# Kernel optimization log

Hardware: AMD Instinct MI355X
Metric: run time of the kernel (lower is better)

Reference implementation:

```python
import jax, jax.numpy as jnp
import numpy as np

N, R, T = 40000, 2000, 500000   # node_size, rel_size, triple_size
D, DEPTH, PROXY_N = 128, 2, 64  # node_F, depth, proxy rows
DC = D * (DEPTH + 1)            # 384


def _unique_edges(rng, n_rows, n_cols, n_edges):
    # sorted, duplicate-free edge list -> matches torch.sparse coalesce() ordering
    keys = np.unique(rng.integers(0, n_rows * n_cols, size=int(n_edges * 1.05), dtype=np.int64))[:n_edges]
    assert keys.shape[0] == n_edges
    return np.stack([keys // n_cols, keys % n_cols], axis=1)


def _init_emb(key, r, c):
    w = jax.random.normal(key, (r, c), dtype=jnp.float32)
    return w / jnp.maximum(jnp.linalg.norm(w, axis=1, keepdims=True), 1e-12)


def setup_inputs() -> dict:
    rng = np.random.default_rng(0)
    adj = jnp.asarray(_unique_edges(rng, N, N, T))                    # [T,2] (src, dst)
    idx = jnp.stack([jnp.arange(T), jnp.asarray(rng.integers(0, R, T, dtype=np.int64))], axis=1)  # [T,2]
    val = jnp.ones((T,), jnp.float32)
    ent_m = jnp.asarray(_unique_edges(rng, N, N, T))
    rel_m = jnp.asarray(_unique_edges(rng, N, R, T))
    ks = jax.random.split(jax.random.key(0), 12)
    return {
        "ent_emb": _init_emb(ks[0], N, D),
        "rel_emb": _init_emb(ks[1], R, D),
        "e_gate": _init_emb(ks[2], DC, DC),
        "e_proxy": _init_emb(ks[3], PROXY_N, DC),
        "e_bias": _init_emb(ks[4], 1, DC),
        "e_attn": jnp.stack([_init_emb(ks[5], D, 1), _init_emb(ks[6], D, 1)]),
        "r_gate": _init_emb(ks[7], DC, DC),
        "r_proxy": _init_emb(ks[8], PROXY_N, DC),
        "r_bias": _init_emb(ks[9], 1, DC),
        "r_attn": jnp.stack([_init_emb(ks[10], D, 1), _init_emb(ks[11], D, 1)]),
        "val_input": val,
        "adj_input": adj,
        "index_input": idx,
        "ent_matrix": ent_m,
        "rel_matrix": rel_m,
    }


def _l2(x):
    return x / jnp.maximum(jnp.linalg.norm(x, axis=-1, keepdims=True), 1e-12)


def _seg_softmax(v, seg, n):
    m = jax.ops.segment_max(v, seg, num_segments=n)
    e = jnp.exp(v - m[seg])
    s = jax.ops.segment_sum(e, seg, num_segments=n)
    return e / s[seg]


def _adj_agg(edges, emb, n_rows):
    # torch.sparse.softmax over rows of an all-ones adjacency, then sparse @ emb
    rows, cols = edges[:, 0], edges[:, 1]
    w = _seg_softmax(jnp.zeros(edges.shape[0], emb.dtype), rows, n_rows)
    return jax.ops.segment_sum(w[:, None] * emb[cols], rows, num_segments=n_rows)


def _graph_attention(features, rel_emb, edges, sp_idx, sp_val, attn, gate_k, proxy, bias):
    n = features.shape[0]
    t = sp_val.shape[0]
    feats = jnp.tanh(features)
    outs = [feats]
    for l in range(DEPTH):
        # sparse (T,R) @ rel_emb -> per-edge relation embedding, then L2 normalize
        rels_sum = _l2(jax.ops.segment_sum(sp_val[:, None] * rel_emb[sp_idx[:, 1]], sp_idx[:, 0], num_segments=t))
        neighs = feats[edges[:, 1]]                                   # [T,D]
        neighs = neighs - 2.0 * jnp.sum(neighs * rels_sum, axis=1, keepdims=True) * rels_sum  # Householder reflection
        att = _seg_softmax((rels_sum @ attn[l])[:, 0], edges[:, 0], n)  # sparse row softmax
        feats = jnp.tanh(jax.ops.segment_sum(neighs * att[:, None], edges[:, 0], num_segments=n))
        outs.append(feats)
    outputs = jnp.concatenate(outs, axis=1)                           # [N, DC]
    pa = jax.nn.softmax(_l2(outputs) @ _l2(proxy).T, axis=-1)         # [N, 64]
    pf = outputs - pa @ proxy
    gate = jax.nn.sigmoid(pf @ gate_k + bias)
    return gate * outputs + (1.0 - gate) * pf


def reference(ent_emb, rel_emb, e_gate, e_proxy, e_bias, e_attn, r_gate, r_proxy, r_bias, r_attn, val_input, adj_input, index_input, ent_matrix, rel_matrix):
    ent_feature = _adj_agg(ent_matrix, ent_emb, N)                    # [N,D]
    rel_feature = _adj_agg(rel_matrix, rel_emb, N)                    # [N,D]
    out_e = _graph_attention(ent_feature, rel_emb, adj_input, index_input, val_input, e_attn, e_gate, e_proxy, e_bias)
    out_r = _graph_attention(rel_feature, rel_emb, adj_input, index_input, val_input, r_attn, r_gate, r_proxy, r_bias)
    # dropout_rate = 0.0 -> identity
    return jnp.concatenate([out_e, out_r], axis=-1)                   # [N, 2*DC]
```

## Files before the change

kernel.cpp:

```cpp
#include <hip/hip_runtime.h>
#include <hip/hip_fp16.h>


typedef __attribute__((ext_vector_type(4))) float f32x4;
typedef _Float16 h16x2 __attribute__((ext_vector_type(2)));
typedef _Float16 f16x8 __attribute__((ext_vector_type(8)));
typedef float f32x16 __attribute__((ext_vector_type(16)));

__device__ __forceinline__ float wave_sum(float v) {
#pragma unroll
  for (int o = 32; o > 0; o >>= 1) v += __shfl_xor(v, o, 64);
  return v;
}
__device__ __forceinline__ float wave_max(float v) {
#pragma unroll
  for (int o = 32; o > 0; o >>= 1) v = fmaxf(v, __shfl_xor(v, o, 64));
  return v;
}
__device__ __forceinline__ unsigned pkhalf2(float a, float b) {
  __half2 h = __floats2half2_rn(a, b);
  return __builtin_bit_cast(unsigned, h);
}
__device__ __forceinline__ float bcf(unsigned u) {
  return __builtin_bit_cast(float, u);
}
__device__ __forceinline__ unsigned short f2h(float x) {
  return __builtin_bit_cast(unsigned short, (_Float16)x);
}
__device__ __forceinline__ float h2f(unsigned short h) {
  return (float)__builtin_bit_cast(_Float16, h);
}
__device__ __forceinline__ float tanh_fast(float x) {
  float t = __expf(-2.f * fabsf(x));
  float y = (1.f - t) / (1.f + t);
  return copysignf(y, x);
}
__device__ __forceinline__ float fdot2u(unsigned a, unsigned b, float c) {
#if __has_builtin(__builtin_amdgcn_fdot2)
  return __builtin_amdgcn_fdot2(__builtin_bit_cast(h16x2, a),
                                __builtin_bit_cast(h16x2, b), c, false);
#else
  h16x2 x = __builtin_bit_cast(h16x2, a), y = __builtin_bit_cast(h16x2, b);
  return fmaf((float)x.x, (float)y.x, fmaf((float)x.y, (float)y.y, c));
#endif
}

__global__ void rowptr3_kernel(const int* __restrict__ e0,
                               const int* __restrict__ e1,
                               const int* __restrict__ e2, int T, int N,
                               int* __restrict__ p0, int* __restrict__ p1,
                               int* __restrict__ p2) {
  int tid = blockIdx.x * blockDim.x + threadIdx.x;
  int which = tid / (N + 1);
  int r = tid - which * (N + 1);
  if (which >= 3) return;
  const int* E = which == 0 ? e0 : (which == 1 ? e1 : e2);
  int* P = which == 0 ? p0 : (which == 1 ? p1 : p2);
  int lo = 0, hi = T;
  while (lo < hi) {
    int mid = (lo + hi) >> 1;
    if (E[2 * mid] < r) lo = mid + 1; else hi = mid;
  }
  P[r] = lo;
}

__global__ void relprep_kernel(const float* __restrict__ rel_emb,
                               const float* __restrict__ e_attn,
                               const float* __restrict__ r_attn, int R,
                               float* __restrict__ srel,
                               unsigned* __restrict__ rnorm,
                               unsigned* __restrict__ rel16) {
  int r = blockIdx.x * 4 + (threadIdx.x >> 6);
  int lane = threadIdx.x & 63;
  if (r >= R) return;
  float2 v  = *(const float2*)(rel_emb + (size_t)r * 128 + 2 * lane);
  float2 a0 = *(const float2*)(e_attn + 2 * lane);
  float2 a1 = *(const float2*)(e_attn + 128 + 2 * lane);
  float2 b0 = *(const float2*)(r_attn + 2 * lane);
  float2 b1 = *(const float2*)(r_attn + 128 + 2 * lane);
  float n  = wave_sum(v.x * v.x + v.y * v.y);
  float d0 = wave_sum(v.x * a0.x + v.y * a0.y);
  float d1 = wave_sum(v.x * a1.x + v.y * a1.y);
  float d2 = wave_sum(v.x * b0.x + v.y * b0.y);
  float d3 = wave_sum(v.x * b1.x + v.y * b1.y);
  float inv = 1.f / fmaxf(sqrtf(n), 1e-12f);
  rnorm[(size_t)r * 64 + lane] = pkhalf2(v.x * inv, v.y * inv);
  rel16[(size_t)r * 64 + lane] = pkhalf2(v.x, v.y);
  if (lane == 0) {
    srel[r]          = d0 * inv;
    srel[R + r]      = d1 * inv;
    srel[2 * R + r]  = d2 * inv;
    srel[3 * R + r]  = d3 * inv;
  }
}

__global__ void pack_f16_kernel(const float* __restrict__ src,
                                unsigned* __restrict__ dst, int n2) {
  int i = blockIdx.x * blockDim.x + threadIdx.x;
  if (i >= n2) return;
  float2 v = *(const float2*)(src + 2 * (size_t)i);
  dst[i] = pkhalf2(v.x, v.y);
}

__global__ __launch_bounds__(256) void stats_kernel(
    const int* __restrict__ ptr, const int* __restrict__ idx,
    const float* __restrict__ srel, int R, float* __restrict__ stats, int N) {
  int r = blockIdx.x * 4 + (threadIdx.x >> 6);
  if (r >= N) return;
  int lane = threadIdx.x & 63;
  int beg = ptr[r], end = ptr[r + 1];
  const float* s0 = srel;
  const float* s1 = srel + R;
  const float* s2 = srel + 2 * R;
  const float* s3 = srel + 3 * R;
  float m0 = -INFINITY, m1 = -INFINITY, m2 = -INFINITY, m3 = -INFINITY;
  for (int e = beg + lane; e < end; e += 64) {
    int rel = idx[2 * e + 1];
    m0 = fmaxf(m0, s0[rel]); m1 = fmaxf(m1, s1[rel]);
    m2 = fmaxf(m2, s2[rel]); m3 = fmaxf(m3, s3[rel]);
  }
#pragma unroll
  for (int o = 32; o > 0; o >>= 1) {
    m0 = fmaxf(m0, __shfl_xor(m0, o, 64));
    m1 = fmaxf(m1, __shfl_xor(m1, o, 64));
    m2 = fmaxf(m2, __shfl_xor(m2, o, 64));
    m3 = fmaxf(m3, __shfl_xor(m3, o, 64));
  }
  float d0 = 0.f, d1 = 0.f, d2 = 0.f, d3 = 0.f;
  for (int e = beg + lane; e < end; e += 64) {
    int rel = idx[2 * e + 1];
    d0 += __expf(s0[rel] - m0); d1 += __expf(s1[rel] - m1);
    d2 += __expf(s2[rel] - m2); d3 += __expf(s3[rel] - m3);
  }
#pragma unroll
  for (int o = 32; o > 0; o >>= 1) {
    d0 += __shfl_xor(d0, o, 64); d1 += __shfl_xor(d1, o, 64);
    d2 += __shfl_xor(d2, o, 64); d3 += __shfl_xor(d3, o, 64);
  }
  if (lane == 0) {
    float4 a, b;
    a.x = m0; a.y = (d0 > 0.f) ? 1.f / d0 : 0.f;
    a.z = m1; a.w = (d1 > 0.f) ? 1.f / d1 : 0.f;
    b.x = m2; b.y = (d2 > 0.f) ? 1.f / d2 : 0.f;
    b.z = m3; b.w = (d3 > 0.f) ? 1.f / d3 : 0.f;
    *(float4*)(stats + (size_t)r * 8) = a;
    *(float4*)(stats + (size_t)r * 8 + 4) = b;
  }
}

__global__ void weight_kernel(const int* __restrict__ adj,
                              const int* __restrict__ idx,
                              const float* __restrict__ srel, int R,
                              const float* __restrict__ stats,
                              unsigned* __restrict__ pk,
                              uint2* __restrict__ wt0,
                              uint2* __restrict__ wt1, int T) {
  int e = blockIdx.x * blockDim.x + threadIdx.x;
  if (e >= T) return;
  int row = adj[2 * e];
  int col = adj[2 * e + 1];
  int rel = idx[2 * e + 1];
  float4 a = *(const float4*)(stats + (size_t)row * 8);
  float4 b = *(const float4*)(stats + (size_t)row * 8 + 4);
  float w0 = __expf(srel[rel] - a.x) * a.y;
  float w1 = __expf(srel[R + rel] - a.z) * a.w;
  float w2 = __expf(srel[2 * R + rel] - b.x) * b.y;
  float w3 = __expf(srel[3 * R + rel] - b.z) * b.w;
  pk[e] = (unsigned)col | ((unsigned)rel << 16);
  wt0[e] = make_uint2(__builtin_bit_cast(unsigned, w0),
                      __builtin_bit_cast(unsigned, w2));
  wt1[e] = make_uint2(__builtin_bit_cast(unsigned, w1),
                      __builtin_bit_cast(unsigned, w3));
}

__global__ __launch_bounds__(256) void agg_fused_kernel(
    const int* __restrict__ ptrE, const int* __restrict__ edgesE,
    const unsigned* __restrict__ ent16, const int* __restrict__ ptrR,
    const int* __restrict__ edgesR, const unsigned* __restrict__ rel16,
    unsigned* __restrict__ fout, int N) {
  int r = blockIdx.x * 4 + (threadIdx.x >> 6);
  if (r >= N) return;
  int lane = threadIdx.x & 63;
  int g = lane >> 4, q = lane & 15;

  float aE[8] = {0, 0, 0, 0, 0, 0, 0, 0};
  float aR[8] = {0, 0, 0, 0, 0, 0, 0, 0};

  auto addh = [&](uint4 u, float* a) {
    h16x2 h0 = __builtin_bit_cast(h16x2, u.x), h1 = __builtin_bit_cast(h16x2, u.y);
    h16x2 h2 = __builtin_bit_cast(h16x2, u.z), h3 = __builtin_bit_cast(h16x2, u.w);
    a[0] += (float)h0.x; a[1] += (float)h0.y;
    a[2] += (float)h1.x; a[3] += (float)h1.y;
    a[4] += (float)h2.x; a[5] += (float)h2.y;
    a[6] += (float)h3.x; a[7] += (float)h3.y;
  };

  int begE = ptrE[r], endE = ptrE[r + 1];
  for (int e0 = begE; e0 < endE; e0 += 8) {
    int eA = e0 + g, eB = e0 + 4 + g;
    if (eA < endE)
      addh(*(const uint4*)(ent16 + (size_t)edgesE[2 * eA + 1] * 64 + 4 * q), aE);
    if (eB < endE)
      addh(*(const uint4*)(ent16 + (size_t)edgesE[2 * eB + 1] * 64 + 4 * q), aE);
  }
  int begR = ptrR[r], endR = ptrR[r + 1];
  for (int e0 = begR; e0 < endR; e0 += 8) {
    int eA = e0 + g, eB = e0 + 4 + g;
    if (eA < endR)
      addh(*(const uint4*)(rel16 + (size_t)edgesR[2 * eA + 1] * 64 + 4 * q), aR);
    if (eB < endR)
      addh(*(const uint4*)(rel16 + (size_t)edgesR[2 * eB + 1] * 64 + 4 * q), aR);
  }
#pragma unroll
  for (int j = 0; j < 8; ++j) {
    aE[j] += __shfl_xor(aE[j], 16, 64); aE[j] += __shfl_xor(aE[j], 32, 64);
    aR[j] += __shfl_xor(aR[j], 16, 64); aR[j] += __shfl_xor(aR[j], 32, 64);
  }
  float sE = (endE > begE) ? 1.f / (float)(endE - begE) : 0.f;
  float sR = (endR > begR) ? 1.f / (float)(endR - begR) : 0.f;
  if (g == 0) {
    float t[8];
#pragma unroll
    for (int j = 0; j < 8; ++j) t[j] = tanh_fast(aE[j] * sE);
    uint4 u;
    u.x = pkhalf2(t[0], t[1]); u.y = pkhalf2(t[2], t[3]);
    u.z = pkhalf2(t[4], t[5]); u.w = pkhalf2(t[6], t[7]);
    *(uint4*)(fout + (size_t)r * 128 + 4 * q) = u;
  } else if (g == 1) {
    float t[8];
#pragma unroll
    for (int j = 0; j < 8; ++j) t[j] = tanh_fast(aR[j] * sR);
    uint4 u;
    u.x = pkhalf2(t[0], t[1]); u.y = pkhalf2(t[2], t[3]);
    u.z = pkhalf2(t[4], t[5]); u.w = pkhalf2(t[6], t[7]);
    *(uint4*)(fout + (size_t)r * 128 + 64 + 4 * q) = u;
  }
}

__global__ __launch_bounds__(256) void layer_rec_kernel(
    const int* __restrict__ ptr, const unsigned* __restrict__ pk,
    const uint2* __restrict__ wt, const unsigned* __restrict__ rnorm,
    const unsigned* __restrict__ fin, unsigned* __restrict__ foutE,
    unsigned* __restrict__ foutR, int fstride, int N) {
  int r = blockIdx.x * 4 + (threadIdx.x >> 6);
  if (r >= N) return;
  int lane = threadIdx.x & 63;
  int g = lane >> 4, q = lane & 15;
  int beg = ptr[r], end = ptr[r + 1];

  float aE[8] = {0, 0, 0, 0, 0, 0, 0, 0};
  float aR[8] = {0, 0, 0, 0, 0, 0, 0, 0};

  auto accum = [&](uint4 F, uint4 V, float w, float s, float* a) {
    h16x2 f0 = __builtin_bit_cast(h16x2, F.x), v0 = __builtin_bit_cast(h16x2, V.x);
    h16x2 f1 = __builtin_bit_cast(h16x2, F.y), v1 = __builtin_bit_cast(h16x2, V.y);
    h16x2 f2 = __builtin_bit_cast(h16x2, F.z), v2 = __builtin_bit_cast(h16x2, V.z);
    h16x2 f3 = __builtin_bit_cast(h16x2, F.w), v3 = __builtin_bit_cast(h16x2, V.w);
    a[0] = fmaf((float)f0.x, w, fmaf((float)v0.x, s, a[0]));
    a[1] = fmaf((float)f0.y, w, fmaf((float)v0.y, s, a[1]));
    a[2] = fmaf((float)f1.x, w, fmaf((float)v1.x, s, a[2]));
    a[3] = fmaf((float)f1.y, w, fmaf((float)v1.y, s, a[3]));
    a[4] = fmaf((float)f2.x, w, fmaf((float)v2.x, s, a[4]));
    a[5] = fmaf((float)f2.y, w, fmaf((float)v2.y, s, a[5]));
    a[6] = fmaf((float)f3.x, w, fmaf((float)v3.x, s, a[6]));
    a[7] = fmaf((float)f3.y, w, fmaf((float)v3.y, s, a[7]));
  };

  for (int e0 = beg; e0 < end; e0 += 8) {
    int eA = e0 + g, eB = e0 + 4 + g;
    bool actA = eA < end, actB = eB < end;
    unsigned pkA = actA ? pk[eA] : 0u;
    unsigned pkB = actB ? pk[eB] : 0u;
    uint2 wA = actA ? wt[eA] : make_uint2(0u, 0u);
    uint2 wB = actB ? wt[eB] : make_uint2(0u, 0u);
    int colA = (int)(pkA & 0xFFFFu), relA = (int)(pkA >> 16);
    int colB = (int)(pkB & 0xFFFFu), relB = (int)(pkB >> 16);
    float wAE = bcf(wA.x), wAR = bcf(wA.y);
    float wBE = bcf(wB.x), wBR = bcf(wB.y);

    const unsigned* fA = fin + (size_t)colA * 128;
    const unsigned* fB = fin + (size_t)colB * 128;
    uint4 EA = *(const uint4*)(fA + 4 * q);
    uint4 RA = *(const uint4*)(fA + 64 + 4 * q);
    uint4 VA = *(const uint4*)(rnorm + (size_t)relA * 64 + 4 * q);
    uint4 EB = *(const uint4*)(fB + 4 * q);
    uint4 RB = *(const uint4*)(fB + 64 + 4 * q);
    uint4 VB = *(const uint4*)(rnorm + (size_t)relB * 64 + 4 * q);

    float dAE = fdot2u(EA.w, VA.w, fdot2u(EA.z, VA.z,
                fdot2u(EA.y, VA.y, fdot2u(EA.x, VA.x, 0.f))));
    float dAR = fdot2u(RA.w, VA.w, fdot2u(RA.z, VA.z,
                fdot2u(RA.y, VA.y, fdot2u(RA.x, VA.x, 0.f))));
    float dBE = fdot2u(EB.w, VB.w, fdot2u(EB.z, VB.z,
                fdot2u(EB.y, VB.y, fdot2u(EB.x, VB.x, 0.f))));
    float dBR = fdot2u(RB.w, VB.w, fdot2u(RB.z, VB.z,
                fdot2u(RB.y, VB.y, fdot2u(RB.x, VB.x, 0.f))));
#pragma unroll
    for (int m = 1; m < 16; m <<= 1) {
      dAE += __shfl_xor(dAE, m, 64);
      dAR += __shfl_xor(dAR, m, 64);
      dBE += __shfl_xor(dBE, m, 64);
      dBR += __shfl_xor(dBR, m, 64);
    }
    float sAE = -2.f * wAE * dAE, sAR = -2.f * wAR * dAR;
    float sBE = -2.f * wBE * dBE, sBR = -2.f * wBR * dBR;
    accum(EA, VA, wAE, sAE, aE);
    accum(RA, VA, wAR, sAR, aR);
    accum(EB, VB, wBE, sBE, aE);
    accum(RB, VB, wBR, sBR, aR);
  }

#pragma unroll
  for (int j = 0; j < 8; ++j) {
    aE[j] += __shfl_xor(aE[j], 16, 64); aE[j] += __shfl_xor(aE[j], 32, 64);
    aR[j] += __shfl_xor(aR[j], 16, 64); aR[j] += __shfl_xor(aR[j], 32, 64);
  }
  if (g == 0) {
    float t[8];
#pragma unroll
    for (int j = 0; j < 8; ++j) t[j] = tanh_fast(aE[j]);
    uint4 u;
    u.x = pkhalf2(t[0], t[1]); u.y = pkhalf2(t[2], t[3]);
    u.z = pkhalf2(t[4], t[5]); u.w = pkhalf2(t[6], t[7]);
    *(uint4*)(foutE + (size_t)r * fstride + 4 * q) = u;
  } else if (g == 1) {
    float t[8];
#pragma unroll
    for (int j = 0; j < 8; ++j) t[j] = tanh_fast(aR[j]);
    uint4 u;
    u.x = pkhalf2(t[0], t[1]); u.y = pkhalf2(t[2], t[3]);
    u.z = pkhalf2(t[4], t[5]); u.w = pkhalf2(t[6], t[7]);
    *(uint4*)(foutR + (size_t)r * fstride + 4 * q) = u;
  }
}

__device__ __forceinline__ void pack_one32(const float* __restrict__ src,
                                           unsigned short* __restrict__ dst,
                                           int NT, int srcld, int mode, int f,
                                           int lane) {
  int kt = f / NT, nt = f % NT;
  int kbase = 16 * kt + 8 * (lane >> 5);
  int n = 32 * nt + (lane & 31);
  unsigned short tmp[8];
#pragma unroll
  for (int j = 0; j < 8; ++j) {
    int k = kbase + j;
    float v = (mode == 0) ? src[(size_t)k * srcld + n] : src[(size_t)n * srcld + k];
    tmp[j] = f2h(v);
  }
  *(uint4*)(dst + ((size_t)f * 64 + lane) * 8) = *(uint4*)tmp;
}
__global__ void pack_all_kernel(const float* eP, const float* eG,
                                const float* rP, const float* rG,
                                unsigned short* b1e, unsigned short* b2e,
                                unsigned short* b3e, unsigned short* b1r,
                                unsigned short* b2r, unsigned short* b3r) {
  int f = blockIdx.x * 4 + (threadIdx.x >> 6);
  int lane = threadIdx.x & 63;
  if (f < 48)       pack_one32(eP, b1e, 2, 384, 1, f, lane);
  else if (f < 96)  pack_one32(eP, b2e, 12, 384, 0, f - 48, lane);
  else if (f < 384) pack_one32(eG, b3e, 12, 384, 0, f - 96, lane);
  else if (f < 432) pack_one32(rP, b1r, 2, 384, 1, f - 384, lane);
  else if (f < 480) pack_one32(rP, b2r, 12, 384, 0, f - 432, lane);
  else if (f < 768) pack_one32(rG, b3r, 12, 384, 0, f - 480, lane);
}

__global__ __launch_bounds__(256) void final_fused_kernel(
    const unsigned* __restrict__ f0, const unsigned* __restrict__ f1,
    const unsigned* __restrict__ outu,
    const unsigned short* __restrict__ B1e, const unsigned short* __restrict__ B2e,
    const unsigned short* __restrict__ B3e, const unsigned short* __restrict__ B1r,
    const unsigned short* __restrict__ B2r, const unsigned short* __restrict__ B3r,
    const float* __restrict__ biasE, const float* __restrict__ biasR,
    float* __restrict__ gout) {
  __shared__ __align__(16) unsigned sOutH[32][204];
  __shared__ __align__(16) float sPa[32][68];
  __shared__ __align__(16) unsigned short sPaH[32][72];
  __shared__ float sInv[32];
  unsigned short* sOutHs = (unsigned short*)&sOutH[0][0];

  const int side = blockIdx.x & 1;
  const int row0 = (blockIdx.x >> 1) * 32;
  const int plane = side ? 64 : 0;
  const unsigned* f2 = outu + (side ? 704 : 0);
  const unsigned short* B1 = side ? B1r : B1e;
  const unsigned short* B2 = side ? B2r : B2e;
  const unsigned short* B3 = side ? B3r : B3e;
  const float* bias = side ? biasR : biasE;
  const int coloff = side ? 384 : 0;

  const int t = threadIdx.x;
  const int w = t >> 6, lane = t & 63;
  const int l31 = lane & 31, l5 = lane >> 5;

  {
    int rloc = t >> 3;
    int c0 = t & 7;
    int rg = row0 + rloc;
    float ss = 0.f;
#pragma unroll
    for (int i = 0; i < 6; ++i) {
      int c = c0 + 8 * i;
      int buf = c >> 4, j = c & 15;
      const unsigned* src;
      if (buf == 0)      src = f0 + (size_t)rg * 128 + plane + 4 * j;
      else if (buf == 1) src = f1 + (size_t)rg * 128 + plane + 4 * j;
      else               src = f2 + (size_t)rg * 768 + 4 * j;
      uint4 u = *(const uint4*)src;
      *(uint4*)&sOutH[rloc][c * 4] = u;
      ss = fdot2u(u.x, u.x, fdot2u(u.y, u.y,
           fdot2u(u.z, u.z, fdot2u(u.w, u.w, ss))));
    }
    ss += __shfl_xor(ss, 1, 64);
    ss += __shfl_xor(ss, 2, 64);
    ss += __shfl_xor(ss, 4, 64);
    if (c0 == 0) sInv[rloc] = 1.f / fmaxf(sqrtf(ss), 1e-12f);
  }
  __syncthreads();

  if (w < 2) {
    int ct = w;
    f32x16 acc = {0.f, 0.f, 0.f, 0.f, 0.f, 0.f, 0.f, 0.f,
                  0.f, 0.f, 0.f, 0.f, 0.f, 0.f, 0.f, 0.f};
#pragma unroll
    for (int kt = 0; kt < 24; ++kt) {
      f16x8 a = __builtin_bit_cast(
          f16x8, *(const uint4*)&sOutH[l31][8 * kt + 4 * l5]);
      f16x8 b = *(const f16x8*)(B1 + ((size_t)(kt * 2 + ct) * 64 + lane) * 8);
      acc = __builtin_amdgcn_mfma_f32_32x32x16_f16(a, b, acc, 0, 0, 0);
    }
#pragma unroll
    for (int reg = 0; reg < 16; ++reg) {
      int row = (reg & 3) + 8 * (reg >> 2) + 4 * l5;
      sPa[row][ct * 32 + l31] = acc[reg] * sInv[row];
    }
  }
  __syncthreads();

  for (int rr = 8 * w; rr < 8 * w + 8; ++rr) {
    float v = sPa[rr][lane];
    float mx = wave_max(v);
    float e = __expf(v - mx);
    float s = wave_sum(e);
    sPaH[rr][lane] = f2h(e / s);
  }
  __syncthreads();

  const int ntb = 3 * w;
  unsigned outv[3][8];
  {
    f32x16 acc2[3];
#pragma unroll
    for (int s = 0; s < 3; ++s)
#pragma unroll
      for (int i = 0; i < 16; ++i) acc2[s][i] = 0.f;
#pragma unroll
    for (int kt = 0; kt < 4; ++kt) {
      f16x8 a = __builtin_bit_cast(
          f16x8, *(const uint4*)&sPaH[l31][16 * kt + 8 * l5]);
#pragma unroll
      for (int s = 0; s < 3; ++s) {
        f16x8 b = *(const f16x8*)(B2 + ((size_t)(kt * 12 + ntb + s) * 64 + lane) * 8);
        acc2[s] = __builtin_amdgcn_mfma_f32_32x32x16_f16(a, b, acc2[s], 0, 0, 0);
      }
    }
#pragma unroll
    for (int s = 0; s < 3; ++s) {
      int col = 32 * (ntb + s) + l31;
#pragma unroll
      for (int p = 0; p < 8; ++p) {
        int ra = ((2 * p) & 3) + 8 * (p >> 1) + 4 * l5;
        unsigned short u0 = sOutHs[ra * 408 + col];
        unsigned short u1 = sOutHs[(ra + 1) * 408 + col];
        outv[s][p] = (unsigned)u0 | ((unsigned)u1 << 16);
        float pf0 = h2f(u0) - acc2[s][2 * p];
        float pf1 = h2f(u1) - acc2[s][2 * p + 1];
        sOutHs[ra * 408 + col] = f2h(pf0);
        sOutHs[(ra + 1) * 408 + col] = f2h(pf1);
      }
    }
  }
  __syncthreads();

  f32x16 acc3[3];
#pragma unroll
  for (int s = 0; s < 3; ++s)
#pragma unroll
    for (int i = 0; i < 16; ++i) acc3[s][i] = 0.f;
#pragma unroll
  for (int kt = 0; kt < 24; ++kt) {
    f16x8 a = __builtin_bit_cast(
        f16x8, *(const uint4*)&sOutH[l31][8 * kt + 4 * l5]);
#pragma unroll
    for (int s = 0; s < 3; ++s) {
      f16x8 b = *(const f16x8*)(B3 + ((size_t)(kt * 12 + ntb + s) * 64 + lane) * 8);
      acc3[s] = __builtin_amdgcn_mfma_f32_32x32x16_f16(a, b, acc3[s], 0, 0, 0);
    }
  }

#pragma unroll
  for (int s = 0; s < 3; ++s) {
    int col = 32 * (ntb + s) + l31;
    float bv = bias[col];
#pragma unroll
    for (int p = 0; p < 8; ++p) {
      int ra = ((2 * p) & 3) + 8 * (p >> 1) + 4 * l5;
      float g0 = 1.f / (1.f + __expf(-(acc3[s][2 * p] + bv)));
      float g1 = 1.f / (1.f + __expf(-(acc3[s][2 * p + 1] + bv)));
      float pf0 = h2f(sOutHs[ra * 408 + col]);
      float pf1 = h2f(sOutHs[(ra + 1) * 408 + col]);
      unsigned ov = outv[s][p];
      float o0 = h2f((unsigned short)(ov & 0xffffu));
      float o1 = h2f((unsigned short)(ov >> 16));
      gout[(size_t)(row0 + ra) * 768 + coloff + col] = g0 * o0 + (1.f - g0) * pf0;
      gout[(size_t)(row0 + ra + 1) * 768 + coloff + col] =
          g1 * o1 + (1.f - g1) * pf1;
    }
  }
}

extern "C" void kernel_launch(void* const* d_in, const int* in_sizes, int n_in,
                              void* d_out, int out_size, void* d_ws,
                              size_t ws_size, hipStream_t stream) {
  (void)n_in; (void)out_size; (void)ws_size;
  const float* ent_emb = (const float*)d_in[0];
  const float* rel_emb = (const float*)d_in[1];
  const float* e_gate  = (const float*)d_in[2];
  const float* e_proxy = (const float*)d_in[3];
  const float* e_bias  = (const float*)d_in[4];
  const float* e_attn  = (const float*)d_in[5];
  const float* r_gate  = (const float*)d_in[6];
  const float* r_proxy = (const float*)d_in[7];
  const float* r_bias  = (const float*)d_in[8];
  const float* r_attn  = (const float*)d_in[9];
  const int* adj   = (const int*)d_in[11];
  const int* idx   = (const int*)d_in[12];
  const int* ent_m = (const int*)d_in[13];
  const int* rel_m = (const int*)d_in[14];
  const int N = in_sizes[0] / 128;
  const int R = in_sizes[1] / 128;
  const int T = in_sizes[10];
  float* out = (float*)d_out;

  char* w = (char*)d_ws;
  size_t used = 0;
  auto alloc = [&](size_t bytes) {
    void* p = (void*)(w + used);
    used += (bytes + 255) & ~(size_t)255;
    return p;
  };
  int* ptr_adj  = (int*)alloc((size_t)(N + 1) * sizeof(int));
  int* ptr_ent  = (int*)alloc((size_t)(N + 1) * sizeof(int));
  int* ptr_rel  = (int*)alloc((size_t)(N + 1) * sizeof(int));
  float* srel   = (float*)alloc((size_t)4 * R * sizeof(float));
  unsigned short* b1e = (unsigned short*)alloc(48 * 1024);
  unsigned short* b2e = (unsigned short*)alloc(48 * 1024);
  unsigned short* b3e = (unsigned short*)alloc(288 * 1024);
  unsigned short* b1r = (unsigned short*)alloc(48 * 1024);
  unsigned short* b2r = (unsigned short*)alloc(48 * 1024);
  unsigned short* b3r = (unsigned short*)alloc(288 * 1024);
  unsigned* rnorm = (unsigned*)alloc((size_t)R * 64 * 4);
  unsigned* rel16 = (unsigned*)alloc((size_t)R * 64 * 4);
  unsigned* ent16 = (unsigned*)alloc((size_t)N * 64 * 4);
  unsigned* fsrc0 = (unsigned*)alloc((size_t)N * 128 * 4);
  unsigned* fsrc1 = (unsigned*)alloc((size_t)N * 128 * 4);
  float* stats = (float*)alloc((size_t)N * 8 * sizeof(float));
  unsigned* pk = (unsigned*)alloc((size_t)T * 4);
  uint2* wt0 = (uint2*)alloc((size_t)T * 8);
  uint2* wt1 = (uint2*)alloc((size_t)T * 8);

  dim3 b256(256);
  rowptr3_kernel<<<(3 * (N + 1) + 255) / 256, b256, 0, stream>>>(
      adj, ent_m, rel_m, T, N, ptr_adj, ptr_ent, ptr_rel);
  relprep_kernel<<<(R + 3) / 4, b256, 0, stream>>>(rel_emb, e_attn, r_attn, R,
                                                   srel, rnorm, rel16);
  pack_f16_kernel<<<(N * 64 + 255) / 256, b256, 0, stream>>>(ent_emb, ent16,
                                                             N * 64);
  pack_all_kernel<<<192, b256, 0, stream>>>(e_proxy, e_gate, r_proxy, r_gate,
                                            b1e, b2e, b3e, b1r, b2r, b3r);

  int grow = (N + 3) / 4;
  stats_kernel<<<grow, b256, 0, stream>>>(ptr_adj, idx, srel, R, stats, N);
  weight_kernel<<<(T + 255) / 256, b256, 0, stream>>>(adj, idx, srel, R, stats,
                                                      pk, wt0, wt1, T);
  agg_fused_kernel<<<grow, b256, 0, stream>>>(ptr_ent, ent_m, ent16, ptr_rel,
                                              rel_m, rel16, fsrc0, N);
  unsigned* outu = (unsigned*)out;
  layer_rec_kernel<<<grow, b256, 0, stream>>>(ptr_adj, pk, wt0, rnorm, fsrc0,
                                              fsrc1, fsrc1 + 64, 128, N);
  layer_rec_kernel<<<grow, b256, 0, stream>>>(ptr_adj, pk, wt1, rnorm, fsrc1,
                                              outu, outu + 704, 768, N);

  int fblocks = 2 * ((N + 31) / 32);
  final_fused_kernel<<<fblocks, b256, 0, stream>>>(
      fsrc0, fsrc1, outu, b1e, b2e, b3e, b1r, b2r, b3r, e_bias, r_bias, out);
}
```

Measured before the change: 293.7 us.

## Drop softmax max pass via precomputed exp, prefetch MFMA B tiles, add occupancy bound

The per-relation attention scores are exponentiated once per relation, so the per-row softmax needs only a sum pass instead of a max pass plus a sum pass. The weight kernel then becomes a multiply of a cached exp by a per-row inverse. Edge packing moves into its own kernel so stats and weights read compact 4-byte edges. The final fused kernel also software-prefetches the B fragments for the next k-step and gets a launch_bounds occupancy hint of 4. Skipping the max subtraction risks overflow for large scores, though scores here are dot products of unit-norm vectors and stay small.

```diff
diff --git a/kernel.cpp b/kernel.cpp
--- a/kernel.cpp
+++ b/kernel.cpp
@@ -43,6 +43,10 @@
   h16x2 x = __builtin_bit_cast(h16x2, a), y = __builtin_bit_cast(h16x2, b);
   return fmaf((float)x.x, (float)y.x, fmaf((float)x.y, (float)y.y, c));
 #endif
+}
+__device__ __forceinline__ float dot8(uint4 a, uint4 b) {
+  return fdot2u(a.w, b.w, fdot2u(a.z, b.z, fdot2u(a.y, b.y,
+         fdot2u(a.x, b.x, 0.f))));
 }
 
 __global__ void rowptr3_kernel(const int* __restrict__ e0,
@@ -67,7 +71,7 @@
 __global__ void relprep_kernel(const float* __restrict__ rel_emb,
                                const float* __restrict__ e_attn,
                                const float* __restrict__ r_attn, int R,
-                               float* __restrict__ srel,
+                               float4* __restrict__ expS4,
                                unsigned* __restrict__ rnorm,
                                unsigned* __restrict__ rel16) {
   int r = blockIdx.x * 4 + (threadIdx.x >> 6);
@@ -87,10 +91,8 @@
   rnorm[(size_t)r * 64 + lane] = pkhalf2(v.x * inv, v.y * inv);
   rel16[(size_t)r * 64 + lane] = pkhalf2(v.x, v.y);
   if (lane == 0) {
-    srel[r]          = d0 * inv;
-    srel[R + r]      = d1 * inv;
-    srel[2 * R + r]  = d2 * inv;
-    srel[3 * R + r]  = d3 * inv;
+    expS4[r] = make_float4(__expf(d0 * inv), __expf(d1 * inv),
+                           __expf(d2 * inv), __expf(d3 * inv));
   }
 }
 
@@ -102,35 +104,25 @@
   dst[i] = pkhalf2(v.x, v.y);
 }
 
-__global__ __launch_bounds__(256) void stats_kernel(
-    const int* __restrict__ ptr, const int* __restrict__ idx,
-    const float* __restrict__ srel, int R, float* __restrict__ stats, int N) {
+__global__ void pack_edges_kernel(const int* __restrict__ adj,
+                                  const int* __restrict__ idx,
+                                  unsigned* __restrict__ pk, int T) {
+  int e = blockIdx.x * blockDim.x + threadIdx.x;
+  if (e >= T) return;
+  pk[e] = (unsigned)adj[2 * e + 1] | ((unsigned)idx[2 * e + 1] << 16);
+}
+
+__global__ __launch_bounds__(256) void stats4_kernel(
+    const int* __restrict__ ptr, const unsigned* __restrict__ pk,
+    const float4* __restrict__ expS4, float4* __restrict__ inv4, int N) {
   int r = blockIdx.x * 4 + (threadIdx.x >> 6);
   if (r >= N) return;
   int lane = threadIdx.x & 63;
   int beg = ptr[r], end = ptr[r + 1];
-  const float* s0 = srel;
-  const float* s1 = srel + R;
-  const float* s2 = srel + 2 * R;
-  const float* s3 = srel + 3 * R;
-  float m0 = -INFINITY, m1 = -INFINITY, m2 = -INFINITY, m3 = -INFINITY;
-  for (int e = beg + lane; e < end; e += 64) {
-    int rel = idx[2 * e + 1];
-    m0 = fmaxf(m0, s0[rel]); m1 = fmaxf(m1, s1[rel]);
-    m2 = fmaxf(m2, s2[rel]); m3 = fmaxf(m3, s3[rel]);
-  }
-#pragma unroll
-  for (int o = 32; o > 0; o >>= 1) {
-    m0 = fmaxf(m0, __shfl_xor(m0, o, 64));
-    m1 = fmaxf(m1, __shfl_xor(m1, o, 64));
-    m2 = fmaxf(m2, __shfl_xor(m2, o, 64));
-    m3 = fmaxf(m3, __shfl_xor(m3, o, 64));
-  }
   float d0 = 0.f, d1 = 0.f, d2 = 0.f, d3 = 0.f;
   for (int e = beg + lane; e < end; e += 64) {
-    int rel = idx[2 * e + 1];
-    d0 += __expf(s0[rel] - m0); d1 += __expf(s1[rel] - m1);
-    d2 += __expf(s2[rel] - m2); d3 += __expf(s3[rel] - m3);
+    float4 es = expS4[pk[e] >> 16];
+    d0 += es.x; d1 += es.y; d2 += es.z; d3 += es.w;
   }
 #pragma unroll
   for (int o = 32; o > 0; o >>= 1) {
@@ -138,39 +130,29 @@
     d2 += __shfl_xor(d2, o, 64); d3 += __shfl_xor(d3, o, 64);
   }
   if (lane == 0) {
-    float4 a, b;
-    a.x = m0; a.y = (d0 > 0.f) ? 1.f / d0 : 0.f;
-    a.z = m1; a.w = (d1 > 0.f) ? 1.f / d1 : 0.f;
-    b.x = m2; b.y = (d2 > 0.f) ? 1.f / d2 : 0.f;
-    b.z = m3; b.w = (d3 > 0.f) ? 1.f / d3 : 0.f;
-    *(float4*)(stats + (size_t)r * 8) = a;
-    *(float4*)(stats + (size_t)r * 8 + 4) = b;
+    inv4[r] = make_float4(d0 > 0.f ? 1.f / d0 : 0.f,
+                          d1 > 0.f ? 1.f / d1 : 0.f,
+                          d2 > 0.f ? 1.f / d2 : 0.f,
+                          d3 > 0.f ? 1.f / d3 : 0.f);
   }
 }
 
 __global__ void weight_kernel(const int* __restrict__ adj,
-                              const int* __restrict__ idx,
-                              const float* __restrict__ srel, int R,
-                              const float* __restrict__ stats,
-                              unsigned* __restrict__ pk,
+                              const unsigned* __restrict__ pk,
+                              const float4* __restrict__ expS4,
+                              const float4* __restrict__ inv4,
                               uint2* __restrict__ wt0,
                               uint2* __restrict__ wt1, int T) {
   int e = blockIdx.x * blockDim.x + threadIdx.x;
   if (e >= T) return;
   int row = adj[2 * e];
-  int col = adj[2 * e + 1];
-  int rel = idx[2 * e + 1];
-  float4 a = *(const float4*)(stats + (size_t)row * 8);
-  float4 b = *(const float4*)(stats + (size_t)row * 8 + 4);
-  float w0 = __expf(srel[rel] - a.x) * a.y;
-  float w1 = __expf(srel[R + rel] - a.z) * a.w;
-  float w2 = __expf(srel[2 * R + rel] - b.x) * b.y;
-  float w3 = __expf(srel[3 * R + rel] - b.z) * b.w;
-  pk[e] = (unsigned)col | ((unsigned)rel << 16);
-  wt0[e] = make_uint2(__builtin_bit_cast(unsigned, w0),
-                      __builtin_bit_cast(unsigned, w2));
-  wt1[e] = make_uint2(__builtin_bit_cast(unsigned, w1),
-                      __builtin_bit_cast(unsigned, w3));
+  int rel = (int)(pk[e] >> 16);
+  float4 es = expS4[rel];
+  float4 iv = inv4[row];
+  wt0[e] = make_uint2(__builtin_bit_cast(unsigned, es.x * iv.x),
+                      __builtin_bit_cast(unsigned, es.z * iv.z));
+  wt1[e] = make_uint2(__builtin_bit_cast(unsigned, es.y * iv.y),
+                      __builtin_bit_cast(unsigned, es.w * iv.w));
 }
 
 __global__ __launch_bounds__(256) void agg_fused_kernel(
@@ -287,14 +269,8 @@
     uint4 RB = *(const uint4*)(fB + 64 + 4 * q);
     uint4 VB = *(const uint4*)(rnorm + (size_t)relB * 64 + 4 * q);
 
-    float dAE = fdot2u(EA.w, VA.w, fdot2u(EA.z, VA.z,
-                fdot2u(EA.y, VA.y, fdot2u(EA.x, VA.x, 0.f))));
-    float dAR = fdot2u(RA.w, VA.w, fdot2u(RA.z, VA.z,
-                fdot2u(RA.y, VA.y, fdot2u(RA.x, VA.x, 0.f))));
-    float dBE = fdot2u(EB.w, VB.w, fdot2u(EB.z, VB.z,
-                fdot2u(EB.y, VB.y, fdot2u(EB.x, VB.x, 0.f))));
-    float dBR = fdot2u(RB.w, VB.w, fdot2u(RB.z, VB.z,
-                fdot2u(RB.y, VB.y, fdot2u(RB.x, VB.x, 0.f))));
+    float dAE = dot8(EA, VA), dAR = dot8(RA, VA);
+    float dBE = dot8(EB, VB), dBR = dot8(RB, VB);
 #pragma unroll
     for (int m = 1; m < 16; m <<= 1) {
       dAE += __shfl_xor(dAE, m, 64);
@@ -365,7 +341,7 @@
   else if (f < 768) pack_one32(rG, b3r, 12, 384, 0, f - 480, lane);
 }
 
-__global__ __launch_bounds__(256) void final_fused_kernel(
+__global__ __launch_bounds__(256, 4) void final_fused_kernel(
     const unsigned* __restrict__ f0, const unsigned* __restrict__ f1,
     const unsigned* __restrict__ outu,
     const unsigned short* __restrict__ B1e, const unsigned short* __restrict__ B2e,
@@ -422,12 +398,16 @@
     int ct = w;
     f32x16 acc = {0.f, 0.f, 0.f, 0.f, 0.f, 0.f, 0.f, 0.f,
                   0.f, 0.f, 0.f, 0.f, 0.f, 0.f, 0.f, 0.f};
+    f16x8 bh = *(const f16x8*)(B1 + ((size_t)ct * 64 + lane) * 8);
 #pragma unroll
     for (int kt = 0; kt < 24; ++kt) {
+      f16x8 bn;
+      if (kt < 23)
+        bn = *(const f16x8*)(B1 + ((size_t)((kt + 1) * 2 + ct) * 64 + lane) * 8);
       f16x8 a = __builtin_bit_cast(
           f16x8, *(const uint4*)&sOutH[l31][8 * kt + 4 * l5]);
-      f16x8 b = *(const f16x8*)(B1 + ((size_t)(kt * 2 + ct) * 64 + lane) * 8);
-      acc = __builtin_amdgcn_mfma_f32_32x32x16_f16(a, b, acc, 0, 0, 0);
+      acc = __builtin_amdgcn_mfma_f32_32x32x16_f16(a, bh, acc, 0, 0, 0);
+      bh = bn;
     }
 #pragma unroll
     for (int reg = 0; reg < 16; ++reg) {
@@ -487,14 +467,24 @@
   for (int s = 0; s < 3; ++s)
 #pragma unroll
     for (int i = 0; i < 16; ++i) acc3[s][i] = 0.f;
-#pragma unroll
-  for (int kt = 0; kt < 24; ++kt) {
-    f16x8 a = __builtin_bit_cast(
-        f16x8, *(const uint4*)&sOutH[l31][8 * kt + 4 * l5]);
-#pragma unroll
-    for (int s = 0; s < 3; ++s) {
-      f16x8 b = *(const f16x8*)(B3 + ((size_t)(kt * 12 + ntb + s) * 64 + lane) * 8);
-      acc3[s] = __builtin_amdgcn_mfma_f32_32x32x16_f16(a, b, acc3[s], 0, 0, 0);
+  {
+    f16x8 bh0 = *(const f16x8*)(B3 + ((size_t)(ntb + 0) * 64 + lane) * 8);
+    f16x8 bh1 = *(const f16x8*)(B3 + ((size_t)(ntb + 1) * 64 + lane) * 8);
+    f16x8 bh2 = *(const f16x8*)(B3 + ((size_t)(ntb + 2) * 64 + lane) * 8);
+#pragma unroll
+    for (int kt = 0; kt < 24; ++kt) {
+      f16x8 bn0, bn1, bn2;
+      if (kt < 23) {
+        bn0 = *(const f16x8*)(B3 + ((size_t)((kt + 1) * 12 + ntb + 0) * 64 + lane) * 8);
+        bn1 = *(const f16x8*)(B3 + ((size_t)((kt + 1) * 12 + ntb + 1) * 64 + lane) * 8);
+        bn2 = *(const f16x8*)(B3 + ((size_t)((kt + 1) * 12 + ntb + 2) * 64 + lane) * 8);
+      }
+      f16x8 a = __builtin_bit_cast(
+          f16x8, *(const uint4*)&sOutH[l31][8 * kt + 4 * l5]);
+      acc3[0] = __builtin_amdgcn_mfma_f32_32x32x16_f16(a, bh0, acc3[0], 0, 0, 0);
+      acc3[1] = __builtin_amdgcn_mfma_f32_32x32x16_f16(a, bh1, acc3[1], 0, 0, 0);
+      acc3[2] = __builtin_amdgcn_mfma_f32_32x32x16_f16(a, bh2, acc3[2], 0, 0, 0);
+      bh0 = bn0; bh1 = bn1; bh2 = bn2;
     }
   }
 
@@ -552,7 +542,6 @@
   int* ptr_adj  = (int*)alloc((size_t)(N + 1) * sizeof(int));
   int* ptr_ent  = (int*)alloc((size_t)(N + 1) * sizeof(int));
   int* ptr_rel  = (int*)alloc((size_t)(N + 1) * sizeof(int));
-  float* srel   = (float*)alloc((size_t)4 * R * sizeof(float));
   unsigned short* b1e = (unsigned short*)alloc(48 * 1024);
   unsigned short* b2e = (unsigned short*)alloc(48 * 1024);
   unsigned short* b3e = (unsigned short*)alloc(288 * 1024);
@@ -564,7 +553,8 @@
   unsigned* ent16 = (unsigned*)alloc((size_t)N * 64 * 4);
   unsigned* fsrc0 = (unsigned*)alloc((size_t)N * 128 * 4);
   unsigned* fsrc1 = (unsigned*)alloc((size_t)N * 128 * 4);
-  float* stats = (float*)alloc((size_t)N * 8 * sizeof(float));
+  float4* expS4 = (float4*)alloc((size_t)R * 16);
+  float4* inv4  = (float4*)alloc((size_t)N * 16);
   unsigned* pk = (unsigned*)alloc((size_t)T * 4);
   uint2* wt0 = (uint2*)alloc((size_t)T * 8);
   uint2* wt1 = (uint2*)alloc((size_t)T * 8);
@@ -573,16 +563,17 @@
   rowptr3_kernel<<<(3 * (N + 1) + 255) / 256, b256, 0, stream>>>(
       adj, ent_m, rel_m, T, N, ptr_adj, ptr_ent, ptr_rel);
   relprep_kernel<<<(R + 3) / 4, b256, 0, stream>>>(rel_emb, e_attn, r_attn, R,
-                                                   srel, rnorm, rel16);
+                                                   expS4, rnorm, rel16);
   pack_f16_kernel<<<(N * 64 + 255) / 256, b256, 0, stream>>>(ent_emb, ent16,
                                                              N * 64);
+  pack_edges_kernel<<<(T + 255) / 256, b256, 0, stream>>>(adj, idx, pk, T);
   pack_all_kernel<<<192, b256, 0, stream>>>(e_proxy, e_gate, r_proxy, r_gate,
                                             b1e, b2e, b3e, b1r, b2r, b3r);
 
   int grow = (N + 3) / 4;
-  stats_kernel<<<grow, b256, 0, stream>>>(ptr_adj, idx, srel, R, stats, N);
-  weight_kernel<<<(T + 255) / 256, b256, 0, stream>>>(adj, idx, srel, R, stats,
-                                                      pk, wt0, wt1, T);
+  stats4_kernel<<<grow, b256, 0, stream>>>(ptr_adj, pk, expS4, inv4, N);
+  weight_kernel<<<(T + 255) / 256, b256, 0, stream>>>(adj, pk, expS4, inv4,
+                                                      wt0, wt1, T);
   agg_fused_kernel<<<grow, b256, 0, stream>>>(ptr_ent, ent_m, ent16, ptr_rel,
                                               rel_m, rel16, fsrc0, N);
   unsigned* outu = (unsigned*)out;
```

Measured after the change: 305.7 us. 1.04x slower.
